# Kernel optimization log

Hardware: AMD Instinct MI355X
Metric: run time of the kernel (lower is better)

The kernel has to match this reference:

```python
import jax, jax.numpy as jnp
import numpy as np
from jax import lax

MAXW = 4  # spans cover j in [i, min(i+4, max_len)) -> widths 1..4


def setup_inputs() -> dict:
    key = jax.random.key(0)
    ks = jax.random.split(key, 8)
    B, L, H = 64, 512, 256
    Hd = H // 2  # dynamicLSTM hidden = kernel_num/2
    s = 0.05
    feats = jax.random.normal(ks[0], (B, L, H), dtype=jnp.float32)
    lens = jax.random.randint(ks[1], (B,), 1, L + 1)
    W_ih = jax.random.normal(ks[2], (4 * Hd, H), dtype=jnp.float32) * s
    W_hh = jax.random.normal(ks[3], (4 * Hd, Hd), dtype=jnp.float32) * s
    b_ih = jax.random.normal(ks[4], (4 * Hd,), dtype=jnp.float32) * s
    b_hh = jax.random.normal(ks[5], (4 * Hd,), dtype=jnp.float32) * s
    W_tri = jax.random.normal(ks[6], (2, Hd), dtype=jnp.float32) * s
    b_tri = jax.random.normal(ks[7], (2,), dtype=jnp.float32) * s
    return {"feats": feats, "W_ih": W_ih, "W_hh": W_hh, "b_ih": b_ih,
            "b_hh": b_hh, "W_tri": W_tri, "b_tri": b_tri, "lens": lens}


def _build_tag_graph(feats, W_ih, W_hh, b_ih, b_hh, W_tri, b_tri, lens):
    B, Lmax, H = feats.shape
    Hd = W_hh.shape[1]
    starts = jnp.arange(Lmax)
    idx = starts[:, None] + jnp.arange(MAXW)[None, :]              # (L, 4)
    in_range = idx < Lmax
    win = feats[:, jnp.minimum(idx, Lmax - 1)] * in_range[None, :, :, None]  # (B, L, 4, H)
    x = win.transpose(2, 0, 1, 3).reshape(MAXW, B * Lmax, H)       # steps-major

    def step(carry, xt):
        h, c = carry
        gates = xt @ W_ih.T + b_ih + h @ W_hh.T + b_hh
        i_, f_, g_, o_ = jnp.split(gates, 4, axis=-1)  # torch gate order i,f,g,o
        c = jax.nn.sigmoid(f_) * c + jax.nn.sigmoid(i_) * jnp.tanh(g_)
        h = jax.nn.sigmoid(o_) * jnp.tanh(c)
        return (h, c), h

    h0 = jnp.zeros((B * Lmax, Hd), feats.dtype)
    _, hs = lax.scan(step, (h0, h0), x)                            # (4, B*L, Hd)
    hs = hs.reshape(MAXW, B, Lmax, Hd).transpose(1, 2, 0, 3)       # (B, L, 4, Hd); [...,t,:] = hidden after t+1 steps

    # effective packed length per span: total = clip(lens - i, 0, w); pack uses max(total, 1)
    w = jnp.arange(1, MAXW + 1)                                    # span widths
    rem = lens[:, None] - starts[None, :]                          # (B, L)
    total = jnp.clip(rem[:, :, None], 0, w[None, None, :])         # (B, L, 4)
    Lsel = jnp.maximum(total, 1)
    row_mask = (total > 0).astype(feats.dtype)
    h_span = jnp.take_along_axis(hs, (Lsel - 1)[..., None], axis=2)  # (B, L, 4, Hd)

    emit = (h_span @ W_tri.T + b_tri) * row_mask[..., None]        # (B, L, 4, 2)
    # scatter emit[b, i, w-1] into span_scores[b, i, i+w-1]; drop spans past max_len
    valid_span = in_range  # j = i + (w-1) < Lmax
    emit = emit * valid_span[None, :, :, None]
    j_clamped = jnp.minimum(idx, Lmax - 1)
    span_scores = jnp.zeros((B, Lmax, Lmax, 2), feats.dtype)
    span_scores = span_scores.at[:, starts[:, None], j_clamped].add(emit)
    return span_scores


def reference(feats, W_ih, W_hh, b_ih, b_hh, W_tri, b_tri, lens):
    return _build_tag_graph(feats, W_ih, W_hh, b_ih, b_hh, W_tri, b_tri, lens)
```

## Files before the change

### kernel.cpp

```cpp
#include <hip/hip_runtime.h>
#include <cstddef>

#define NB 64
#define LL 512
#define HH 256
#define HD 128
#define NG 512
#define TI 16

typedef _Float16 half_t;
typedef _Float16 half8 __attribute__((ext_vector_type(8)));
typedef _Float16 half4 __attribute__((ext_vector_type(4)));
typedef float f32x4 __attribute__((ext_vector_type(4)));

#define MFMA16(a, b, c) __builtin_amdgcn_mfma_f32_16x16x32_f16((a), (b), (c), 0, 0, 0)

#define FP 264
#define XP 518
#define HBP 136
#define EP 17

__device__ __forceinline__ float sigm(float x)  { return __builtin_amdgcn_rcpf(1.0f + __expf(-x)); }
__device__ __forceinline__ float tanhf_(float x){ return 2.0f * __builtin_amdgcn_rcpf(1.0f + __expf(-2.0f * x)) - 1.0f; }

template <int CTRL>
__device__ __forceinline__ float dppadd(float x) {
    int v = __builtin_amdgcn_update_dpp(0, __float_as_int(x), CTRL, 0xF, 0xF, true);
    return x + __int_as_float(v);
}
__device__ __forceinline__ float row16_sum(float x) {
    x = dppadd<0xB1>(x);
    x = dppadd<0x4E>(x);
    x = dppadd<0x141>(x);
    x = dppadd<0x140>(x);
    return x;
}

__device__ __forceinline__ void barrier_lgkm() {
    asm volatile("s_waitcnt lgkmcnt(0)" ::: "memory");
    __builtin_amdgcn_s_barrier();
    asm volatile("" ::: "memory");
}

__global__ void prep_weights(const float* __restrict__ Wih, const float* __restrict__ Whh,
                             const float* __restrict__ bih, const float* __restrict__ bhh,
                             half_t* __restrict__ WihH, half_t* __restrict__ WhhH,
                             float* __restrict__ bsum)
{
    const int idx = blockIdx.x * 256 + threadIdx.x;
    if (idx < NG * HH) WihH[idx] = (half_t)Wih[idx];
    if (idx < NG * HD) WhhH[idx] = (half_t)Whh[idx];
    if (idx < NG)      bsum[idx] = bih[idx] + bhh[idx];
}

__global__ __launch_bounds__(512, 4) void span_lstm_mfma(
    const float* __restrict__ feats, const half_t* __restrict__ WihH,
    const half_t* __restrict__ WhhH, const float* __restrict__ bsum,
    const float* __restrict__ W_tri, const float* __restrict__ b_tri,
    const int* __restrict__ lens, float* __restrict__ out)
{
    __shared__ __align__(16) half_t sFeatb[20 * FP];
    __shared__ __align__(16) float  sXG[20 * XP];
    __shared__ __align__(16) half_t sHb[2][16 * HBP];
    __shared__ __align__(16) float  sE[4][16 * EP];

    float* sVal = (float*)sFeatb;

    const int tid = threadIdx.x;
    const int b  = blockIdx.x >> 5;
    const int i0 = (blockIdx.x & 31) * TI;
    const int lens_b = lens[b];

    if (i0 >= lens_b) return;

    float* ob = out + ((size_t)b * LL + i0) * (LL * 2);

    const int lane = tid & 63, wv = tid >> 6;
    const int lm = lane & 15;
    const int lq = lane >> 4;
    const int jw = wv * 16;

    for (int idx = tid; idx < 20 * 64; idx += 512) {
        const int p  = idx >> 6;
        const int k4 = (idx & 63) << 2;
        const int gp = i0 + p;
        float4 v = make_float4(0.f, 0.f, 0.f, 0.f);
        if (gp < LL) v = *(const float4*)(feats + ((size_t)b * LL + gp) * HH + k4);
        half4 hv = {(half_t)v.x, (half_t)v.y, (half_t)v.z, (half_t)v.w};
        *(half4*)(&sFeatb[p * FP + k4]) = hv;
    }
    __syncthreads();

    {
        half8 afr[2][8];
        #pragma unroll
        for (int mt = 0; mt < 2; ++mt)
            #pragma unroll
            for (int kf = 0; kf < 8; ++kf)
                afr[mt][kf] = *(const half8*)(&sFeatb[(16 * mt + lm) * FP + kf * 32 + lq * 8]);

        #pragma unroll
        for (int ta = 0; ta < 4; ++ta) {
            const int gb = ta * HD + jw;
            const float bs = bsum[gb + lm];
            f32x4 acc0 = {0.f, 0.f, 0.f, 0.f}, acc1 = {0.f, 0.f, 0.f, 0.f};
            #pragma unroll
            for (int kf = 0; kf < 8; ++kf) {
                const half8 bfr = *(const half8*)(WihH + (size_t)(gb + lm) * HH + kf * 32 + lq * 8);
                acc0 = MFMA16(afr[0][kf], bfr, acc0);
                acc1 = MFMA16(afr[1][kf], bfr, acc1);
            }
            #pragma unroll
            for (int r = 0; r < 4; ++r)
                sXG[(lq * 4 + r) * XP + gb + lm] = acc0[r] + bs;
            if (lq == 0) {
                #pragma unroll
                for (int r = 0; r < 4; ++r)
                    sXG[(16 + r) * XP + gb + lm] = acc1[r] + bs;
            }
        }
    }

    half8 bf2[4][4];
    #pragma unroll
    for (int ta = 0; ta < 4; ++ta)
        #pragma unroll
        for (int kf = 0; kf < 4; ++kf)
            bf2[ta][kf] = *(const half8*)(WhhH + (size_t)(ta * HD + jw + lm) * HD
                                          + kf * 32 + lq * 8);
    const float wt0 = W_tri[jw + lm];
    const float wt1 = W_tri[HD + jw + lm];
    const float bt0 = b_tri[0], bt1 = b_tri[1];

    float cc4[4] = {0.f, 0.f, 0.f, 0.f};
    float hhA[4][4];

    #pragma unroll
    for (int t = 0; t < 4; ++t) {
        float accg[4][4];
        if (t > 0) {
            half8 ah[4];
            #pragma unroll
            for (int kf = 0; kf < 4; ++kf)
                ah[kf] = *(const half8*)(&sHb[(t - 1) & 1][lm * HBP + kf * 32 + lq * 8]);
            #pragma unroll
            for (int ta = 0; ta < 4; ++ta) {
                f32x4 a = {0.f, 0.f, 0.f, 0.f};
                #pragma unroll
                for (int kf = 0; kf < 4; ++kf)
                    a = MFMA16(ah[kf], bf2[ta][kf], a);
                #pragma unroll
                for (int r = 0; r < 4; ++r) accg[ta][r] = a[r];
            }
        } else {
            #pragma unroll
            for (int ta = 0; ta < 4; ++ta)
                #pragma unroll
                for (int r = 0; r < 4; ++r) accg[ta][r] = 0.f;
        }
        #pragma unroll
        for (int ta = 0; ta < 4; ++ta)
            #pragma unroll
            for (int r = 0; r < 4; ++r)
                accg[ta][r] += sXG[(lq * 4 + r + t) * XP + ta * HD + jw + lm];

        #pragma unroll
        for (int r = 0; r < 4; ++r) {
            const float ig = sigm(accg[0][r]);
            const float fg = sigm(accg[1][r]);
            const float gg = tanhf_(accg[2][r]);
            const float og = sigm(accg[3][r]);
            cc4[r] = fg * cc4[r] + ig * gg;
            hhA[t][r] = og * tanhf_(cc4[r]);
        }

        if (t < 3) {
            #pragma unroll
            for (int r = 0; r < 4; ++r)
                sHb[t & 1][(lq * 4 + r) * HBP + jw + lm] = (half_t)hhA[t][r];
            barrier_lgkm();
        }
    }

    #pragma unroll
    for (int ts = 0; ts < 4; ++ts)
        #pragma unroll
        for (int r = 0; r < 4; ++r) {
            float e0 = row16_sum(hhA[ts][r] * wt0);
            float e1 = row16_sum(hhA[ts][r] * wt1);
            if (lm == 0) {
                float2 v = make_float2(e0, e1);
                *(float2*)&sE[ts][(lq * 4 + r) * EP + wv * 2] = v;
            }
        }
    barrier_lgkm();

    if (tid < 128) {
        const int es = tid & 15, tag = (tid >> 4) & 1, w = (tid >> 5) + 1;
        const int i = i0 + es;
        const int rem = lens_b - i;
        float e = 0.f;
        if (rem > 0 && (i + w - 1) < LL) {
            const int ts = (rem < w ? rem : w) - 1;
            e = tag ? bt1 : bt0;
            #pragma unroll
            for (int k = 0; k < 8; ++k) e += sE[ts][es * EP + k * 2 + tag];
        }
        sVal[(es * 4 + (w - 1)) * 2 + tag] = e;
    }
    barrier_lgkm();

    if (tid < 48) {
        const int es = tid & 15, m = tid >> 4;
        const int i = i0 + es;
        if (i < lens_b) {
            const int chi = ((i + 3 < LL) ? (i + 3) : (LL - 1)) >> 1;
            const int c = (i >> 1) + m;
            if (c <= chi) {
                const int j0 = 2 * c;
                f32x4 v = {0.f, 0.f, 0.f, 0.f};
                const int w0 = j0 - i + 1;
                if ((unsigned)(w0 - 1) < 4u) {
                    v.x = sVal[(es * 4 + (w0 - 1)) * 2 + 0];
                    v.y = sVal[(es * 4 + (w0 - 1)) * 2 + 1];
                }
                const int w1 = w0 + 1;
                if ((unsigned)(w1 - 1) < 4u) {
                    v.z = sVal[(es * 4 + (w1 - 1)) * 2 + 0];
                    v.w = sVal[(es * 4 + (w1 - 1)) * 2 + 1];
                }
                *(f32x4*)(ob + ((size_t)es * 256 + c) * 4) = v;
            }
        }
    }
}

extern "C" void kernel_launch(void* const* d_in, const int* in_sizes, int n_in,
                              void* d_out, int out_size, void* d_ws, size_t ws_size,
                              hipStream_t stream)
{
    const float* feats = (const float*)d_in[0];
    const float* W_ih  = (const float*)d_in[1];
    const float* W_hh  = (const float*)d_in[2];
    const float* b_ih  = (const float*)d_in[3];
    const float* b_hh  = (const float*)d_in[4];
    const float* W_tri = (const float*)d_in[5];
    const float* b_tri = (const float*)d_in[6];
    const int*   lens  = (const int*)d_in[7];
    float* out = (float*)d_out;

    hipMemsetAsync(out, 0, (size_t)out_size * sizeof(float), stream);

    half_t* WihH = (half_t*)d_ws;
    half_t* WhhH = WihH + (size_t)NG * HH;
    float*  bsum = (float*)(WhhH + (size_t)NG * HD);

    prep_weights<<<(NG * HH + 255) / 256, 256, 0, stream>>>(W_ih, W_hh, b_ih, b_hh,
                                                            WihH, WhhH, bsum);
    span_lstm_mfma<<<NB * (LL / TI), 512, 0, stream>>>(feats, WihH, WhhH, bsum,
                                                       W_tri, b_tri, lens, out);
}
```

Baseline: 258.1 us.

## Process two batch rows per block to reuse weight fragments

Each block now handles the same 16-start tile for two batch entries. The input-projection GEMM packs the 19 needed rows of each batch into three MFMA M-tiles instead of four. Recurrent W_hh fragments held in registers are shared across both batches. This halves global weight loads per output and cuts the wasted MFMA rows. In exchange, registers and LDS per block double, launch bounds drop to 2 blocks per CU, and early exit now only happens when both batch lengths are exceeded, so some padded work returns.

After: 253.0 us. -2.0%, faster.

```diff
diff --git a/kernel.cpp b/kernel.cpp
--- a/kernel.cpp
+++ b/kernel.cpp
@@ -53,70 +53,90 @@
     if (idx < NG)      bsum[idx] = bih[idx] + bhh[idx];
 }
 
-__global__ __launch_bounds__(512, 4) void span_lstm_mfma(
+__global__ __launch_bounds__(512, 2) void span_lstm_mfma(
     const float* __restrict__ feats, const half_t* __restrict__ WihH,
     const half_t* __restrict__ WhhH, const float* __restrict__ bsum,
     const float* __restrict__ W_tri, const float* __restrict__ b_tri,
     const int* __restrict__ lens, float* __restrict__ out)
 {
-    __shared__ __align__(16) half_t sFeatb[20 * FP];
-    __shared__ __align__(16) float  sXG[20 * XP];
-    __shared__ __align__(16) half_t sHb[2][16 * HBP];
-    __shared__ __align__(16) float  sE[4][16 * EP];
+    __shared__ __align__(16) half_t sFeatb[40 * FP];
+    __shared__ __align__(16) float  sXG[2][19 * XP];
+    __shared__ __align__(16) half_t sHb[2][32 * HBP];
+    __shared__ __align__(16) float  sE[4][32 * EP];
 
     float* sVal = (float*)sFeatb;
 
     const int tid = threadIdx.x;
-    const int b  = blockIdx.x >> 5;
-    const int i0 = (blockIdx.x & 31) * TI;
-    const int lens_b = lens[b];
-
-    if (i0 >= lens_b) return;
-
-    float* ob = out + ((size_t)b * LL + i0) * (LL * 2);
+    const int it = blockIdx.x >> 5;
+    const int q  = blockIdx.x & 31;
+    const int i0 = it * TI;
+    const int b0 = 2 * q, b1 = 2 * q + 1;
+    const int l0 = lens[b0], l1 = lens[b1];
+    const int lmax = l0 > l1 ? l0 : l1;
+    if (i0 >= lmax) return;
 
     const int lane = tid & 63, wv = tid >> 6;
     const int lm = lane & 15;
     const int lq = lane >> 4;
     const int jw = wv * 16;
-
-    for (int idx = tid; idx < 20 * 64; idx += 512) {
+    const int gcol = jw + lm;
+
+    for (int idx = tid; idx < 40 * 64; idx += 512) {
         const int p  = idx >> 6;
         const int k4 = (idx & 63) << 2;
-        const int gp = i0 + p;
+        const int bb = (p >= 20);
+        const int pr = p - bb * 20;
+        const int gp = i0 + pr;
         float4 v = make_float4(0.f, 0.f, 0.f, 0.f);
-        if (gp < LL) v = *(const float4*)(feats + ((size_t)b * LL + gp) * HH + k4);
+        if (gp < LL) v = *(const float4*)(feats + ((size_t)(2 * q + bb) * LL + gp) * HH + k4);
         half4 hv = {(half_t)v.x, (half_t)v.y, (half_t)v.z, (half_t)v.w};
         *(half4*)(&sFeatb[p * FP + k4]) = hv;
     }
     __syncthreads();
 
     {
-        half8 afr[2][8];
-        #pragma unroll
-        for (int mt = 0; mt < 2; ++mt)
-            #pragma unroll
-            for (int kf = 0; kf < 8; ++kf)
-                afr[mt][kf] = *(const half8*)(&sFeatb[(16 * mt + lm) * FP + kf * 32 + lq * 8]);
-
+        float bs[4];
+        #pragma unroll
+        for (int ta = 0; ta < 4; ++ta) bs[ta] = bsum[ta * HD + gcol];
+
+        const int m2row = (lm < 4) ? (16 + lm) : ((lm < 8) ? (32 + lm) : lm);
+
+        f32x4 acc[3][4];
+        #pragma unroll
+        for (int mt = 0; mt < 3; ++mt)
+            #pragma unroll
+            for (int ta = 0; ta < 4; ++ta) acc[mt][ta] = (f32x4){0.f, 0.f, 0.f, 0.f};
+
+        #pragma unroll
+        for (int kf = 0; kf < 8; ++kf) {
+            const half8 a0 = *(const half8*)(&sFeatb[lm * FP        + kf * 32 + lq * 8]);
+            const half8 a1 = *(const half8*)(&sFeatb[(20 + lm) * FP + kf * 32 + lq * 8]);
+            const half8 a2 = *(const half8*)(&sFeatb[m2row * FP     + kf * 32 + lq * 8]);
+            #pragma unroll
+            for (int ta = 0; ta < 4; ++ta) {
+                const half8 bfr = *(const half8*)(WihH + (size_t)(ta * HD + gcol) * HH + kf * 32 + lq * 8);
+                acc[0][ta] = MFMA16(a0, bfr, acc[0][ta]);
+                acc[1][ta] = MFMA16(a1, bfr, acc[1][ta]);
+                acc[2][ta] = MFMA16(a2, bfr, acc[2][ta]);
+            }
+        }
         #pragma unroll
         for (int ta = 0; ta < 4; ++ta) {
-            const int gb = ta * HD + jw;
-            const float bs = bsum[gb + lm];
-            f32x4 acc0 = {0.f, 0.f, 0.f, 0.f}, acc1 = {0.f, 0.f, 0.f, 0.f};
-            #pragma unroll
-            for (int kf = 0; kf < 8; ++kf) {
-                const half8 bfr = *(const half8*)(WihH + (size_t)(gb + lm) * HH + kf * 32 + lq * 8);
-                acc0 = MFMA16(afr[0][kf], bfr, acc0);
-                acc1 = MFMA16(afr[1][kf], bfr, acc1);
-            }
-            #pragma unroll
-            for (int r = 0; r < 4; ++r)
-                sXG[(lq * 4 + r) * XP + gb + lm] = acc0[r] + bs;
+            const int col = ta * HD + gcol;
+            #pragma unroll
+            for (int r = 0; r < 4; ++r) {
+                sXG[0][(lq * 4 + r) * XP + col] = acc[0][ta][r] + bs[ta];
+                sXG[1][(lq * 4 + r) * XP + col] = acc[1][ta][r] + bs[ta];
+            }
             if (lq == 0) {
                 #pragma unroll
-                for (int r = 0; r < 4; ++r)
-                    sXG[(16 + r) * XP + gb + lm] = acc1[r] + bs;
+                for (int r = 0; r < 3; ++r)
+                    sXG[0][(16 + r) * XP + col] = acc[2][ta][r] + bs[ta];
+            }
+            if (lq == 1) {
+                #pragma unroll
+                for (int r = 0; r < 3; ++r)
+                    sXG[1][(16 + r) * XP + col] = acc[2][ta][r] + bs[ta];
             }
         }
     }
@@ -126,58 +146,69 @@
     for (int ta = 0; ta < 4; ++ta)
         #pragma unroll
         for (int kf = 0; kf < 4; ++kf)
-            bf2[ta][kf] = *(const half8*)(WhhH + (size_t)(ta * HD + jw + lm) * HD
-                                          + kf * 32 + lq * 8);
-    const float wt0 = W_tri[jw + lm];
-    const float wt1 = W_tri[HD + jw + lm];
+            bf2[ta][kf] = *(const half8*)(WhhH + (size_t)(ta * HD + gcol) * HD + kf * 32 + lq * 8);
+    const float wt0 = W_tri[gcol];
+    const float wt1 = W_tri[HD + gcol];
     const float bt0 = b_tri[0], bt1 = b_tri[1];
 
-    float cc4[4] = {0.f, 0.f, 0.f, 0.f};
-    float hhA[4][4];
+    float cc4[2][4] = {{0.f,0.f,0.f,0.f},{0.f,0.f,0.f,0.f}};
+    float hhA[4][2][4];
 
     #pragma unroll
     for (int t = 0; t < 4; ++t) {
-        float accg[4][4];
+        float accg[2][4][4];
         if (t > 0) {
-            half8 ah[4];
-            #pragma unroll
-            for (int kf = 0; kf < 4; ++kf)
-                ah[kf] = *(const half8*)(&sHb[(t - 1) & 1][lm * HBP + kf * 32 + lq * 8]);
+            half8 ah0[4], ah1[4];
+            #pragma unroll
+            for (int kf = 0; kf < 4; ++kf) {
+                ah0[kf] = *(const half8*)(&sHb[(t - 1) & 1][lm * HBP        + kf * 32 + lq * 8]);
+                ah1[kf] = *(const half8*)(&sHb[(t - 1) & 1][(16 + lm) * HBP + kf * 32 + lq * 8]);
+            }
             #pragma unroll
             for (int ta = 0; ta < 4; ++ta) {
-                f32x4 a = {0.f, 0.f, 0.f, 0.f};
-                #pragma unroll
-                for (int kf = 0; kf < 4; ++kf)
-                    a = MFMA16(ah[kf], bf2[ta][kf], a);
-                #pragma unroll
-                for (int r = 0; r < 4; ++r) accg[ta][r] = a[r];
+                f32x4 a0 = {0.f,0.f,0.f,0.f}, a1 = {0.f,0.f,0.f,0.f};
+                #pragma unroll
+                for (int kf = 0; kf < 4; ++kf) {
+                    a0 = MFMA16(ah0[kf], bf2[ta][kf], a0);
+                    a1 = MFMA16(ah1[kf], bf2[ta][kf], a1);
+                }
+                #pragma unroll
+                for (int r = 0; r < 4; ++r) { accg[0][ta][r] = a0[r]; accg[1][ta][r] = a1[r]; }
             }
         } else {
             #pragma unroll
+            for (int bb = 0; bb < 2; ++bb)
+                #pragma unroll
+                for (int ta = 0; ta < 4; ++ta)
+                    #pragma unroll
+                    for (int r = 0; r < 4; ++r) accg[bb][ta][r] = 0.f;
+        }
+        #pragma unroll
+        for (int bb = 0; bb < 2; ++bb)
+            #pragma unroll
             for (int ta = 0; ta < 4; ++ta)
                 #pragma unroll
-                for (int r = 0; r < 4; ++r) accg[ta][r] = 0.f;
-        }
-        #pragma unroll
-        for (int ta = 0; ta < 4; ++ta)
-            #pragma unroll
-            for (int r = 0; r < 4; ++r)
-                accg[ta][r] += sXG[(lq * 4 + r + t) * XP + ta * HD + jw + lm];
-
-        #pragma unroll
-        for (int r = 0; r < 4; ++r) {
-            const float ig = sigm(accg[0][r]);
-            const float fg = sigm(accg[1][r]);
-            const float gg = tanhf_(accg[2][r]);
-            const float og = sigm(accg[3][r]);
-            cc4[r] = fg * cc4[r] + ig * gg;
-            hhA[t][r] = og * tanhf_(cc4[r]);
-        }
+                for (int r = 0; r < 4; ++r)
+                    accg[bb][ta][r] += sXG[bb][(lq * 4 + r + t) * XP + ta * HD + gcol];
+
+        #pragma unroll
+        for (int bb = 0; bb < 2; ++bb)
+            #pragma unroll
+            for (int r = 0; r < 4; ++r) {
+                const float ig = sigm(accg[bb][0][r]);
+                const float fg = sigm(accg[bb][1][r]);
+                const float gg = tanhf_(accg[bb][2][r]);
+                const float og = sigm(accg[bb][3][r]);
+                cc4[bb][r] = fg * cc4[bb][r] + ig * gg;
+                hhA[t][bb][r] = og * tanhf_(cc4[bb][r]);
+            }
 
         if (t < 3) {
             #pragma unroll
-            for (int r = 0; r < 4; ++r)
-                sHb[t & 1][(lq * 4 + r) * HBP + jw + lm] = (half_t)hhA[t][r];
+            for (int bb = 0; bb < 2; ++bb)
+                #pragma unroll
+                for (int r = 0; r < 4; ++r)
+                    sHb[t & 1][(bb * 16 + lq * 4 + r) * HBP + gcol] = (half_t)hhA[t][bb][r];
             barrier_lgkm();
         }
     }
@@ -185,35 +216,42 @@
     #pragma unroll
     for (int ts = 0; ts < 4; ++ts)
         #pragma unroll
-        for (int r = 0; r < 4; ++r) {
-            float e0 = row16_sum(hhA[ts][r] * wt0);
-            float e1 = row16_sum(hhA[ts][r] * wt1);
-            if (lm == 0) {
-                float2 v = make_float2(e0, e1);
-                *(float2*)&sE[ts][(lq * 4 + r) * EP + wv * 2] = v;
-            }
-        }
+        for (int bb = 0; bb < 2; ++bb)
+            #pragma unroll
+            for (int r = 0; r < 4; ++r) {
+                float e0 = row16_sum(hhA[ts][bb][r] * wt0);
+                float e1 = row16_sum(hhA[ts][bb][r] * wt1);
+                if (lm == 0) {
+                    float2 v = make_float2(e0, e1);
+                    *(float2*)&sE[ts][(bb * 16 + lq * 4 + r) * EP + wv * 2] = v;
+                }
+            }
     barrier_lgkm();
 
-    if (tid < 128) {
-        const int es = tid & 15, tag = (tid >> 4) & 1, w = (tid >> 5) + 1;
+    if (tid < 256) {
+        const int es = tid & 15, tag = (tid >> 4) & 1, w = ((tid >> 5) & 3) + 1, bb = tid >> 7;
+        const int lb = bb ? l1 : l0;
         const int i = i0 + es;
-        const int rem = lens_b - i;
+        const int rem = lb - i;
         float e = 0.f;
         if (rem > 0 && (i + w - 1) < LL) {
             const int ts = (rem < w ? rem : w) - 1;
             e = tag ? bt1 : bt0;
             #pragma unroll
-            for (int k = 0; k < 8; ++k) e += sE[ts][es * EP + k * 2 + tag];
-        }
-        sVal[(es * 4 + (w - 1)) * 2 + tag] = e;
+            for (int k = 0; k < 8; ++k) e += sE[ts][(bb * 16 + es) * EP + k * 2 + tag];
+        }
+        sVal[((bb * 16 + es) * 4 + (w - 1)) * 2 + tag] = e;
     }
     barrier_lgkm();
 
-    if (tid < 48) {
-        const int es = tid & 15, m = tid >> 4;
+    if (tid < 96) {
+        const int bb = (tid >= 48);
+        const int r2 = tid - bb * 48;
+        const int es = r2 & 15, m = r2 >> 4;
+        const int lb = bb ? l1 : l0;
         const int i = i0 + es;
-        if (i < lens_b) {
+        if (i < lb) {
+            float* obb = out + ((size_t)(2 * q + bb) * LL + i0) * (LL * 2);
             const int chi = ((i + 3 < LL) ? (i + 3) : (LL - 1)) >> 1;
             const int c = (i >> 1) + m;
             if (c <= chi) {
@@ -221,15 +259,15 @@
                 f32x4 v = {0.f, 0.f, 0.f, 0.f};
                 const int w0 = j0 - i + 1;
                 if ((unsigned)(w0 - 1) < 4u) {
-                    v.x = sVal[(es * 4 + (w0 - 1)) * 2 + 0];
-                    v.y = sVal[(es * 4 + (w0 - 1)) * 2 + 1];
+                    v.x = sVal[((bb * 16 + es) * 4 + (w0 - 1)) * 2 + 0];
+                    v.y = sVal[((bb * 16 + es) * 4 + (w0 - 1)) * 2 + 1];
                 }
                 const int w1 = w0 + 1;
                 if ((unsigned)(w1 - 1) < 4u) {
-                    v.z = sVal[(es * 4 + (w1 - 1)) * 2 + 0];
-                    v.w = sVal[(es * 4 + (w1 - 1)) * 2 + 1];
+                    v.z = sVal[((bb * 16 + es) * 4 + (w1 - 1)) * 2 + 0];
+                    v.w = sVal[((bb * 16 + es) * 4 + (w1 - 1)) * 2 + 1];
                 }
-                *(f32x4*)(ob + ((size_t)es * 256 + c) * 4) = v;
+                *(f32x4*)(obb + ((size_t)es * 256 + c) * 4) = v;
             }
         }
     }
@@ -257,6 +295,6 @@
 
     prep_weights<<<(NG * HH + 255) / 256, 256, 0, stream>>>(W_ih, W_hh, b_ih, b_hh,
                                                             WihH, WhhH, bsum);
-    span_lstm_mfma<<<NB * (LL / TI), 512, 0, stream>>>(feats, WihH, WhhH, bsum,
-                                                       W_tri, b_tri, lens, out);
-}
+    span_lstm_mfma<<<(LL / TI) * (NB / 2), 512, 0, stream>>>(feats, WihH, WhhH, bsum,
+                                                             W_tri, b_tri, lens, out);
+}
```
